# Optimization experiments

Hardware: AMD Instinct MI355X
Metric: run time of the kernel (lower is better)

The kernel has to match this reference:

```python
import jax, jax.numpy as jnp
import numpy as np
import math

B, L, D, H = 8, 1000, 1024, 16
HD = D // H

def setup_inputs() -> dict:
    key = jax.random.key(0)
    k1, k2, k3 = jax.random.split(key, 3)
    s_in = 1.0 / math.sqrt(D)
    x = jax.random.normal(k1, (B, L, D), dtype=jnp.float32)
    Wqkv = jax.random.normal(k2, (D, 3 * D), dtype=jnp.float32) * s_in
    bqkv = jnp.zeros((3 * D,), dtype=jnp.float32)
    Wo = jax.random.normal(k3, (D, D), dtype=jnp.float32) * s_in
    bo = jnp.zeros((D,), dtype=jnp.float32)
    return {"x": x, "Wqkv": Wqkv, "bqkv": bqkv, "Wo": Wo, "bo": bo}

def reference(x, Wqkv, bqkv, Wo, bo):
    b, l, d = x.shape
    qkv = x @ Wqkv + bqkv                      # [B,L,3D]
    q, k, v = jnp.split(qkv, 3, axis=-1)       # each [B,L,D]
    q = q.reshape(b, l, H, HD)
    k = k.reshape(b, l, H, HD)
    v = v.reshape(b, l, H, HD)
    scale = 1.0 / math.sqrt(HD)
    att = jnp.einsum('blhd,bmhd->bhlm', q, k) * scale   # [B,H,L,L]
    causal = jnp.tril(jnp.ones((l, l), dtype=bool))      # [L,L]
    att = jnp.where(causal[None, None, :, :], att, -jnp.inf)
    att = jax.nn.softmax(att, axis=-1)
    out = jnp.einsum('bhlm,bmhd->blhd', att, v).reshape(b, l, d)
    return out @ Wo + bo
```

## Files before the change

### kernel.cpp

```cpp
#include <hip/hip_runtime.h>
#include <hip/hip_bf16.h>

typedef unsigned short u16;
typedef unsigned int u32;
typedef __attribute__((ext_vector_type(8))) __bf16 bf16x8;
typedef __attribute__((ext_vector_type(4))) float f32x4;
typedef __attribute__((ext_vector_type(4))) u16 u16x4;

#define LQ 1000
#define MM 8000

__device__ __forceinline__ u16 f2bf(float f){
  __bf16 h = (__bf16)f;
  return __builtin_bit_cast(u16, h);
}
__device__ __forceinline__ void async_copy16(const void* g, void* l){
  __builtin_amdgcn_global_load_lds((const __attribute__((address_space(1))) u32*)g,
                                   (__attribute__((address_space(3))) u32*)l, 16, 0, 0);
}

__device__ __forceinline__ void ttile(const float* __restrict__ src, u16* __restrict__ dst,
                                      int R, int C, int bxt, int byt, u16 (*tile)[33]){
  const int tx = threadIdx.x & 31, ty = threadIdx.x >> 5;
  const long bx = (long)bxt * 32, by = (long)byt * 32;
  #pragma unroll
  for (int i = 0; i < 32; i += 8) tile[ty + i][tx] = f2bf(src[(by + ty + i) * C + bx + tx]);
  __syncthreads();
  #pragma unroll
  for (int i = 0; i < 32; i += 8) dst[(bx + ty + i) * R + by + tx] = tile[tx][ty + i];
}

__global__ __launch_bounds__(256)
void kprep(const float* __restrict__ x, u16* __restrict__ xb,
           const float* __restrict__ Wqkv, u16* __restrict__ WqkvT,
           const float* __restrict__ Wo, u16* __restrict__ WoT)
{
  __shared__ u16 tile[32][33];
  const int bid = blockIdx.x;
  if (bid < 2048) {
    const int t = threadIdx.x;
    for (long base = (long)bid * 1024; base < 8192000L; base += 2048L * 1024) {
      const long i = base + t * 4;
      const float4 v = *(const float4*)&x[i];
      u16x4 o; o.x = f2bf(v.x); o.y = f2bf(v.y); o.z = f2bf(v.z); o.w = f2bf(v.w);
      *(u16x4*)&xb[i] = o;
    }
  } else if (bid < 5120) {
    const int idx = bid - 2048;
    ttile(Wqkv, WqkvT, 1024, 3072, idx % 96, idx / 96, tile);
  } else {
    const int idx = bid - 5120;
    ttile(Wo, WoT, 1024, 1024, idx % 32, idx / 32, tile);
  }
}

template<int EPI, int BN>
__global__ __launch_bounds__(256)
void gemm128(const u16* __restrict__ A, const u16* __restrict__ BT, const float* __restrict__ bias,
             u16* __restrict__ O0, u16* __restrict__ O1, u16* __restrict__ O2,
             float* __restrict__ OF)
{
  constexpr int K = 1024;
  constexpr int NF = BN / 32;
  __shared__ __align__(16) u16 As[2][128 * 32];
  __shared__ __align__(16) u16 Bs[2][BN * 32];
  const int t = threadIdx.x, lane = t & 63, wave = t >> 6;
  const int quad = lane >> 4, l15 = lane & 15;
  const int m0 = blockIdx.y * 128, n0 = blockIdx.x * BN;
  const int wm = (wave >> 1) * 64, wn = (wave & 1) * (BN / 2);

  f32x4 acc[4][NF] = {};

  const int srow = t >> 2;
  const int sg   = (t & 3) ^ ((srow >> 1) & 3);
  const int scol = sg * 8;
  const long aoff0 = (long)min(m0 + srow,      MM - 1) * K + scol;
  const long aoff1 = (long)min(m0 + srow + 64, MM - 1) * K + scol;
  const long boff0 = (long)(n0 + srow)      * K + scol;
  const long boff1 = (long)(n0 + srow + 64) * K + scol;
  char* AsB0 = (char*)As[0] + wave * 1024;
  char* AsB1 = (char*)As[1] + wave * 1024;
  char* BsB0 = (char*)Bs[0] + wave * 1024;
  char* BsB1 = (char*)Bs[1] + wave * 1024;

  const int swz = (l15 >> 1) & 3;

  for (int kt = 0; kt < K; kt += 64) {
    __syncthreads();
    async_copy16(A  + aoff0 + kt,      AsB0);
    async_copy16(A  + aoff1 + kt,      AsB0 + 4096);
    async_copy16(BT + boff0 + kt,      BsB0);
    if constexpr (BN == 128) async_copy16(BT + boff1 + kt,      BsB0 + 4096);
    async_copy16(A  + aoff0 + kt + 32, AsB1);
    async_copy16(A  + aoff1 + kt + 32, AsB1 + 4096);
    async_copy16(BT + boff0 + kt + 32, BsB1);
    if constexpr (BN == 128) async_copy16(BT + boff1 + kt + 32, BsB1 + 4096);
    __syncthreads();
    #pragma unroll
    for (int half = 0; half < 2; half++) {
      bf16x8 af[4], bfv[NF];
      #pragma unroll
      for (int i = 0; i < 4; i++)  af[i]  = *(const bf16x8*)&As[half][(wm + i * 16 + l15) * 32 + (quad ^ swz) * 8];
      #pragma unroll
      for (int i = 0; i < NF; i++) bfv[i] = *(const bf16x8*)&Bs[half][(wn + i * 16 + l15) * 32 + (quad ^ swz) * 8];
      #pragma unroll
      for (int mi = 0; mi < 4; mi++)
        #pragma unroll
        for (int ni = 0; ni < NF; ni++)
          acc[mi][ni] = __builtin_amdgcn_mfma_f32_16x16x32_bf16(af[mi], bfv[ni], acc[mi][ni], 0, 0, 0);
    }
  }

  float bs[NF]; int cols[NF];
  #pragma unroll
  for (int ni = 0; ni < NF; ni++) { cols[ni] = n0 + wn + ni * 16 + l15; bs[ni] = bias[cols[ni]]; }

  #pragma unroll
  for (int mi = 0; mi < 4; mi++) {
    #pragma unroll
    for (int r = 0; r < 4; r++) {
      const int row = m0 + wm + mi * 16 + quad * 4 + r;
      if (row >= MM) continue;
      if (EPI == 0) {
        const int b = row / 1000, l = row - b * 1000;
        #pragma unroll
        for (int ni = 0; ni < NF; ni++) {
          const u16 o = f2bf(acc[mi][ni][r] + bs[ni]);
          const int col = cols[ni];
          const int which = col >> 10, hh = (col >> 6) & 15, dd = col & 63;
          const int bh = b * 16 + hh;
          if      (which == 0) O0[((long)bh * LQ + l) * 64 + dd] = o;
          else if (which == 1) O1[((long)bh * LQ + l) * 64 + dd] = o;
          else                 O2[((long)bh * 64 + dd) * LQ + l] = o;
        }
      } else {
        #pragma unroll
        for (int ni = 0; ni < NF; ni++)
          OF[(long)row * 1024 + cols[ni]] = acc[mi][ni][r] + bs[ni];
      }
    }
  }
}

__global__ __launch_bounds__(256)
void attn_kernel(const u16* __restrict__ Qb, const u16* __restrict__ Kb,
                 const u16* __restrict__ VTb, u16* __restrict__ AO)
{
  __shared__ __align__(16) u16 Ps[4][2][16 * 40];
  const int t = threadIdx.x, lane = t & 63, wave = t >> 6;
  const int quad = lane >> 4, l15 = lane & 15;
  const int lin = blockIdx.y * 4 + blockIdx.x;
  const int swz = (lin & 7) * 64 + (lin >> 3);
  const int bh  = swz >> 2;
  const int c   = (swz & 3) * 4 + wave;
  const u16* Q  = Qb  + (long)bh * LQ * 64;
  const u16* Kp = Kb  + (long)bh * LQ * 64;
  const u16* VT = VTb + (long)bh * 64 * LQ;
  const int b = bh >> 4, h = bh & 15;
  const float sscale = 0.18033688011112042f;

  for (int pass = 0; pass < 2; ++pass) {
    const int chunk = pass ? (31 - c) : c;
    const int qbase = chunk * 32;
    const int nkt = chunk + 1;

    int qv[2]; bf16x8 bq0[2], bq1[2];
    #pragma unroll
    for (int g = 0; g < 2; g++) {
      qv[g] = qbase + g * 16 + l15;
      const int qc = min(qv[g], LQ - 1);
      bq0[g] = *(const bf16x8*)&Q[(long)qc * 64 +      quad * 8];
      bq1[g] = *(const bf16x8*)&Q[(long)qc * 64 + 32 + quad * 8];
    }

    float l_p[2] = { 0.f, 0.f };
    f32x4 o[2][4] = {};

    bf16x8 pa00, pa01, pa10, pa11, pav0, pav1, pav2, pav3;
    {
      const int krA = min(l15, LQ - 1), krB = min(16 + l15, LQ - 1);
      pa00 = *(const bf16x8*)&Kp[(long)krA * 64 +      quad * 8];
      pa01 = *(const bf16x8*)&Kp[(long)krA * 64 + 32 + quad * 8];
      pa10 = *(const bf16x8*)&Kp[(long)krB * 64 +      quad * 8];
      pa11 = *(const bf16x8*)&Kp[(long)krB * 64 + 32 + quad * 8];
      const int vcol = min(quad * 8, LQ - 8);
      pav0 = *(const bf16x8*)&VT[(long)( 0 + l15) * LQ + vcol];
      pav1 = *(const bf16x8*)&VT[(long)(16 + l15) * LQ + vcol];
      pav2 = *(const bf16x8*)&VT[(long)(32 + l15) * LQ + vcol];
      pav3 = *(const bf16x8*)&VT[(long)(48 + l15) * LQ + vcol];
    }

    for (int kk = 0; kk < nkt; ++kk) {
      const int k0 = kk * 32;
      const bool lastt = (kk + 1 == nkt);
      const bf16x8 a00 = pa00, a01 = pa01, a10 = pa10, a11 = pa11;
      bf16x8 av[4] = { pav0, pav1, pav2, pav3 };
      if (!lastt) {
        const int n0k = k0 + 32;
        const int krA = min(n0k + l15, LQ - 1), krB = min(n0k + 16 + l15, LQ - 1);
        pa00 = *(const bf16x8*)&Kp[(long)krA * 64 +      quad * 8];
        pa01 = *(const bf16x8*)&Kp[(long)krA * 64 + 32 + quad * 8];
        pa10 = *(const bf16x8*)&Kp[(long)krB * 64 +      quad * 8];
        pa11 = *(const bf16x8*)&Kp[(long)krB * 64 + 32 + quad * 8];
        const int vcol = min(n0k + quad * 8, LQ - 8);
        pav0 = *(const bf16x8*)&VT[(long)( 0 + l15) * LQ + vcol];
        pav1 = *(const bf16x8*)&VT[(long)(16 + l15) * LQ + vcol];
        pav2 = *(const bf16x8*)&VT[(long)(32 + l15) * LQ + vcol];
        pav3 = *(const bf16x8*)&VT[(long)(48 + l15) * LQ + vcol];
      }

      #pragma unroll
      for (int g = 0; g < 2; g++) {
        const f32x4 z = {};
        __builtin_amdgcn_s_setprio(1);
        f32x4 s0 = __builtin_amdgcn_mfma_f32_16x16x32_bf16(a00, bq0[g], z, 0, 0, 0);
        s0       = __builtin_amdgcn_mfma_f32_16x16x32_bf16(a01, bq1[g], s0, 0, 0, 0);
        f32x4 s1 = __builtin_amdgcn_mfma_f32_16x16x32_bf16(a10, bq0[g], z, 0, 0, 0);
        s1       = __builtin_amdgcn_mfma_f32_16x16x32_bf16(a11, bq1[g], s1, 0, 0, 0);
        __builtin_amdgcn_s_setprio(0);

        float p0[4], p1[4];
        if (lastt) {
          const int q = qv[g];
          #pragma unroll
          for (int r = 0; r < 4; r++) {
            const int key0 = k0 + quad * 4 + r;
            p0[r] = __builtin_amdgcn_exp2f((key0      <= q) ? s0[r] * sscale : -3.0e38f);
            p1[r] = __builtin_amdgcn_exp2f((key0 + 16 <= q) ? s1[r] * sscale : -3.0e38f);
          }
        } else {
          #pragma unroll
          for (int r = 0; r < 4; r++) {
            p0[r] = __builtin_amdgcn_exp2f(s0[r] * sscale);
            p1[r] = __builtin_amdgcn_exp2f(s1[r] * sscale);
          }
        }
        u16x4 w0, w1; float ls = 0.f;
        #pragma unroll
        for (int r = 0; r < 4; r++) {
          w0[r] = f2bf(p0[r]); w1[r] = f2bf(p1[r]);
          ls += p0[r] + p1[r];
        }
        l_p[g] += ls;
        *(u16x4*)&Ps[wave][g][l15 * 40 + quad * 4]      = w0;
        *(u16x4*)&Ps[wave][g][l15 * 40 + 16 + quad * 4] = w1;
        const bf16x8 bp = *(const bf16x8*)&Ps[wave][g][l15 * 40 + quad * 8];
        __builtin_amdgcn_s_setprio(1);
        #pragma unroll
        for (int cc = 0; cc < 4; cc++)
          o[g][cc] = __builtin_amdgcn_mfma_f32_16x16x32_bf16(av[cc], bp, o[g][cc], 0, 0, 0);
        __builtin_amdgcn_s_setprio(0);
      }
    }

    #pragma unroll
    for (int g = 0; g < 2; g++) {
      if (qv[g] >= LQ) continue;
      float l = l_p[g];
      l += __shfl_xor(l, 16);
      l += __shfl_xor(l, 32);
      const float inv = 1.0f / l;
      const long base = ((long)(b * LQ + qv[g])) * 1024 + h * 64;
      #pragma unroll
      for (int cc = 0; cc < 4; cc++) {
        u16x4 w;
        #pragma unroll
        for (int r = 0; r < 4; r++) w[r] = f2bf(o[g][cc][r] * inv);
        *(u16x4*)&AO[base + cc * 16 + quad * 4] = w;
      }
    }
  }
}

extern "C" void kernel_launch(void* const* d_in, const int* in_sizes, int n_in,
                              void* d_out, int out_size, void* d_ws, size_t ws_size,
                              hipStream_t stream) {
  const float* x    = (const float*)d_in[0];
  const float* Wqkv = (const float*)d_in[1];
  const float* bqkv = (const float*)d_in[2];
  const float* Wo   = (const float*)d_in[3];
  const float* bo   = (const float*)d_in[4];
  float* out = (float*)d_out;

  char* ws = (char*)d_ws;
  u16* WqkvT = (u16*)(ws);
  u16* WoT   = (u16*)(ws + 6291456);
  u16* xb    = (u16*)(ws + 8388608);
  u16* Qb    = (u16*)(ws + 8388608 + 16384000L);
  u16* Kb    = (u16*)(ws + 8388608 + 2 * 16384000L);
  u16* VTb   = (u16*)(ws + 8388608 + 3 * 16384000L);
  u16* AO    = xb;

  kprep<<<6144, 256, 0, stream>>>(x, xb, Wqkv, WqkvT, Wo, WoT);
  gemm128<0, 128><<<dim3(24, 63), 256, 0, stream>>>(xb, WqkvT, bqkv, Qb, Kb, VTb, nullptr);
  attn_kernel<<<dim3(4, 128), 256, 0, stream>>>(Qb, Kb, VTb, AO);
  gemm128<1, 64><<<dim3(16, 63), 256, 0, stream>>>(AO, WoT, bo, nullptr, nullptr, nullptr, out);
}
```

Before: 259.9 us.

## Fuse paired causal query chunks into one K/V sweep and widen output GEMM tile

Result: faster. 244.9 us (-5.8%).

```diff
diff --git a/kernel.cpp b/kernel.cpp
--- a/kernel.cpp
+++ b/kernel.cpp
@@ -152,76 +152,80 @@
   const int lin = blockIdx.y * 4 + blockIdx.x;
   const int swz = (lin & 7) * 64 + (lin >> 3);
   const int bh  = swz >> 2;
-  const int c   = (swz & 3) * 4 + wave;
+  const int s   = swz & 3;
+  const int c   = ((wave & 2) ? 8 : 0) + ((wave & 1) ? (7 - s) : s);
+  const int ch[2] = { c, 31 - c };
+  const int nkt = 32 - c;
   const u16* Q  = Qb  + (long)bh * LQ * 64;
   const u16* Kp = Kb  + (long)bh * LQ * 64;
   const u16* VT = VTb + (long)bh * 64 * LQ;
   const int b = bh >> 4, h = bh & 15;
   const float sscale = 0.18033688011112042f;
 
-  for (int pass = 0; pass < 2; ++pass) {
-    const int chunk = pass ? (31 - c) : c;
-    const int qbase = chunk * 32;
-    const int nkt = chunk + 1;
-
-    int qv[2]; bf16x8 bq0[2], bq1[2];
+  int qv[2][2]; bf16x8 bq0[2][2], bq1[2][2];
+  #pragma unroll
+  for (int cj = 0; cj < 2; cj++) {
     #pragma unroll
     for (int g = 0; g < 2; g++) {
-      qv[g] = qbase + g * 16 + l15;
-      const int qc = min(qv[g], LQ - 1);
-      bq0[g] = *(const bf16x8*)&Q[(long)qc * 64 +      quad * 8];
-      bq1[g] = *(const bf16x8*)&Q[(long)qc * 64 + 32 + quad * 8];
-    }
-
-    float l_p[2] = { 0.f, 0.f };
-    f32x4 o[2][4] = {};
-
-    bf16x8 pa00, pa01, pa10, pa11, pav0, pav1, pav2, pav3;
-    {
-      const int krA = min(l15, LQ - 1), krB = min(16 + l15, LQ - 1);
+      qv[cj][g] = ch[cj] * 32 + g * 16 + l15;
+      const int qc = min(qv[cj][g], LQ - 1);
+      bq0[cj][g] = *(const bf16x8*)&Q[(long)qc * 64 +      quad * 8];
+      bq1[cj][g] = *(const bf16x8*)&Q[(long)qc * 64 + 32 + quad * 8];
+    }
+  }
+
+  float l_p[2][2] = {{0.f, 0.f}, {0.f, 0.f}};
+  f32x4 o[2][2][4] = {};
+
+  bf16x8 pa00, pa01, pa10, pa11, pav0, pav1, pav2, pav3;
+  {
+    const int krA = min(l15, LQ - 1), krB = min(16 + l15, LQ - 1);
+    pa00 = *(const bf16x8*)&Kp[(long)krA * 64 +      quad * 8];
+    pa01 = *(const bf16x8*)&Kp[(long)krA * 64 + 32 + quad * 8];
+    pa10 = *(const bf16x8*)&Kp[(long)krB * 64 +      quad * 8];
+    pa11 = *(const bf16x8*)&Kp[(long)krB * 64 + 32 + quad * 8];
+    const int vcol = min(quad * 8, LQ - 8);
+    pav0 = *(const bf16x8*)&VT[(long)( 0 + l15) * LQ + vcol];
+    pav1 = *(const bf16x8*)&VT[(long)(16 + l15) * LQ + vcol];
+    pav2 = *(const bf16x8*)&VT[(long)(32 + l15) * LQ + vcol];
+    pav3 = *(const bf16x8*)&VT[(long)(48 + l15) * LQ + vcol];
+  }
+
+  for (int kk = 0; kk < nkt; ++kk) {
+    const int k0 = kk * 32;
+    const bf16x8 a00 = pa00, a01 = pa01, a10 = pa10, a11 = pa11;
+    bf16x8 av[4] = { pav0, pav1, pav2, pav3 };
+    if (kk + 1 < nkt) {
+      const int n0k = k0 + 32;
+      const int krA = min(n0k + l15, LQ - 1), krB = min(n0k + 16 + l15, LQ - 1);
       pa00 = *(const bf16x8*)&Kp[(long)krA * 64 +      quad * 8];
       pa01 = *(const bf16x8*)&Kp[(long)krA * 64 + 32 + quad * 8];
       pa10 = *(const bf16x8*)&Kp[(long)krB * 64 +      quad * 8];
       pa11 = *(const bf16x8*)&Kp[(long)krB * 64 + 32 + quad * 8];
-      const int vcol = min(quad * 8, LQ - 8);
+      const int vcol = min(n0k + quad * 8, LQ - 8);
       pav0 = *(const bf16x8*)&VT[(long)( 0 + l15) * LQ + vcol];
       pav1 = *(const bf16x8*)&VT[(long)(16 + l15) * LQ + vcol];
       pav2 = *(const bf16x8*)&VT[(long)(32 + l15) * LQ + vcol];
       pav3 = *(const bf16x8*)&VT[(long)(48 + l15) * LQ + vcol];
     }
 
-    for (int kk = 0; kk < nkt; ++kk) {
-      const int k0 = kk * 32;
-      const bool lastt = (kk + 1 == nkt);
-      const bf16x8 a00 = pa00, a01 = pa01, a10 = pa10, a11 = pa11;
-      bf16x8 av[4] = { pav0, pav1, pav2, pav3 };
-      if (!lastt) {
-        const int n0k = k0 + 32;
-        const int krA = min(n0k + l15, LQ - 1), krB = min(n0k + 16 + l15, LQ - 1);
-        pa00 = *(const bf16x8*)&Kp[(long)krA * 64 +      quad * 8];
-        pa01 = *(const bf16x8*)&Kp[(long)krA * 64 + 32 + quad * 8];
-        pa10 = *(const bf16x8*)&Kp[(long)krB * 64 +      quad * 8];
-        pa11 = *(const bf16x8*)&Kp[(long)krB * 64 + 32 + quad * 8];
-        const int vcol = min(n0k + quad * 8, LQ - 8);
-        pav0 = *(const bf16x8*)&VT[(long)( 0 + l15) * LQ + vcol];
-        pav1 = *(const bf16x8*)&VT[(long)(16 + l15) * LQ + vcol];
-        pav2 = *(const bf16x8*)&VT[(long)(32 + l15) * LQ + vcol];
-        pav3 = *(const bf16x8*)&VT[(long)(48 + l15) * LQ + vcol];
-      }
-
+    #pragma unroll
+    for (int cj = 0; cj < 2; cj++) {
+      if (cj == 0 && kk > ch[0]) continue;
+      const bool lastt = (kk == ch[cj]);
       #pragma unroll
       for (int g = 0; g < 2; g++) {
         const f32x4 z = {};
         __builtin_amdgcn_s_setprio(1);
-        f32x4 s0 = __builtin_amdgcn_mfma_f32_16x16x32_bf16(a00, bq0[g], z, 0, 0, 0);
-        s0       = __builtin_amdgcn_mfma_f32_16x16x32_bf16(a01, bq1[g], s0, 0, 0, 0);
-        f32x4 s1 = __builtin_amdgcn_mfma_f32_16x16x32_bf16(a10, bq0[g], z, 0, 0, 0);
-        s1       = __builtin_amdgcn_mfma_f32_16x16x32_bf16(a11, bq1[g], s1, 0, 0, 0);
+        f32x4 s0 = __builtin_amdgcn_mfma_f32_16x16x32_bf16(a00, bq0[cj][g], z, 0, 0, 0);
+        s0       = __builtin_amdgcn_mfma_f32_16x16x32_bf16(a01, bq1[cj][g], s0, 0, 0, 0);
+        f32x4 s1 = __builtin_amdgcn_mfma_f32_16x16x32_bf16(a10, bq0[cj][g], z, 0, 0, 0);
+        s1       = __builtin_amdgcn_mfma_f32_16x16x32_bf16(a11, bq1[cj][g], s1, 0, 0, 0);
         __builtin_amdgcn_s_setprio(0);
 
         float p0[4], p1[4];
         if (lastt) {
-          const int q = qv[g];
+          const int q = qv[cj][g];
           #pragma unroll
           for (int r = 0; r < 4; r++) {
             const int key0 = k0 + quad * 4 + r;
@@ -241,31 +245,34 @@
           w0[r] = f2bf(p0[r]); w1[r] = f2bf(p1[r]);
           ls += p0[r] + p1[r];
         }
-        l_p[g] += ls;
+        l_p[cj][g] += ls;
         *(u16x4*)&Ps[wave][g][l15 * 40 + quad * 4]      = w0;
         *(u16x4*)&Ps[wave][g][l15 * 40 + 16 + quad * 4] = w1;
         const bf16x8 bp = *(const bf16x8*)&Ps[wave][g][l15 * 40 + quad * 8];
         __builtin_amdgcn_s_setprio(1);
         #pragma unroll
         for (int cc = 0; cc < 4; cc++)
-          o[g][cc] = __builtin_amdgcn_mfma_f32_16x16x32_bf16(av[cc], bp, o[g][cc], 0, 0, 0);
+          o[cj][g][cc] = __builtin_amdgcn_mfma_f32_16x16x32_bf16(av[cc], bp, o[cj][g][cc], 0, 0, 0);
         __builtin_amdgcn_s_setprio(0);
       }
     }
-
+  }
+
+  #pragma unroll
+  for (int cj = 0; cj < 2; cj++) {
     #pragma unroll
     for (int g = 0; g < 2; g++) {
-      if (qv[g] >= LQ) continue;
-      float l = l_p[g];
+      if (qv[cj][g] >= LQ) continue;
+      float l = l_p[cj][g];
       l += __shfl_xor(l, 16);
       l += __shfl_xor(l, 32);
       const float inv = 1.0f / l;
-      const long base = ((long)(b * LQ + qv[g])) * 1024 + h * 64;
+      const long base = ((long)(b * LQ + qv[cj][g])) * 1024 + h * 64;
       #pragma unroll
       for (int cc = 0; cc < 4; cc++) {
         u16x4 w;
         #pragma unroll
-        for (int r = 0; r < 4; r++) w[r] = f2bf(o[g][cc][r] * inv);
+        for (int r = 0; r < 4; r++) w[r] = f2bf(o[cj][g][cc][r] * inv);
         *(u16x4*)&AO[base + cc * 16 + quad * 4] = w;
       }
     }
@@ -294,5 +301,5 @@
   kprep<<<6144, 256, 0, stream>>>(x, xb, Wqkv, WqkvT, Wo, WoT);
   gemm128<0, 128><<<dim3(24, 63), 256, 0, stream>>>(xb, WqkvT, bqkv, Qb, Kb, VTb, nullptr);
   attn_kernel<<<dim3(4, 128), 256, 0, stream>>>(Qb, Kb, VTb, AO);
-  gemm128<1, 64><<<dim3(16, 63), 256, 0, stream>>>(AO, WoT, bo, nullptr, nullptr, nullptr, out);
-}
+  gemm128<1, 128><<<dim3(8, 63), 256, 0, stream>>>(AO, WoT, bo, nullptr, nullptr, nullptr, out);
+}
```
